# Kernel optimization log

Hardware: AMD Instinct MI355X
Metric: run time of the kernel (lower is better)

The kernel has to match this reference:

```python
import jax, jax.numpy as jnp
import numpy as np

T, K, E, D, F = 2048, 6, 32, 2048, 1408   # tokens, top_k, routed experts, dim, moe_inter_dim
S = 2                                      # fused shared experts
C = T * K // E                             # exact per-expert capacity (balanced routing)


def _silu_and_mul(gu):
    # merged gate_up activation: silu(gate_half) * up_half
    g, u = jnp.split(gu, 2, axis=-1)
    return jax.nn.silu(g) * u


def setup_inputs() -> dict:
    key = jax.random.key(0)
    ks = jax.random.split(key, 7)
    x = jax.random.normal(ks[0], (T, D), dtype=jnp.float32)
    # balanced routing: every expert receives exactly C = T*K/E token-expert pairs
    indices = jax.random.permutation(ks[1], jnp.arange(T * K, dtype=jnp.int32) % E).reshape(T, K)
    weights = jax.random.uniform(ks[2], (T, K), dtype=jnp.float32)
    scale = 0.02
    w_gate_up = jax.random.normal(ks[3], (E, D, 2 * F), dtype=jnp.float32) * scale
    w_down = jax.random.normal(ks[4], (E, F, D), dtype=jnp.float32) * scale
    w_gate_up_shared = jax.random.normal(ks[5], (S, D, 2 * F), dtype=jnp.float32) * scale
    w_down_shared = jax.random.normal(ks[6], (S, F, D), dtype=jnp.float32) * scale
    return {"x": x, "weights": weights, "w_gate_up": w_gate_up, "w_down": w_down,
            "w_gate_up_shared": w_gate_up_shared, "w_down_shared": w_down_shared,
            "indices": indices}


def reference(x, weights, w_gate_up, w_down, w_gate_up_shared, w_down_shared, indices):
    # ---- dispatch: sort token-expert pairs by expert id (balanced -> exactly C per expert)
    flat_e = indices.reshape(-1)                       # [T*K]
    order = jnp.argsort(flat_e, stable=True)           # [T*K] pair ids grouped by expert
    tok = order // K                                   # source token of each sorted pair
    w_sorted = weights.reshape(-1)[order]              # routing weight of each sorted pair
    xg = x[tok].reshape(E, C, D)                       # gathered per-expert inputs
    # ---- routed experts: grouped gate_up GEMM -> silu_and_mul -> down GEMM
    act = _silu_and_mul(jnp.einsum('ecd,edf->ecf', xg, w_gate_up))   # [E, C, F]
    down = jnp.einsum('ecf,efd->ecd', act, w_down)                   # [E, C, D]
    # ---- combine: weighted scatter-add back to token order (y[idx] += out * weights[idx, top])
    y = jnp.zeros_like(x).at[tok].add(down.reshape(E * C, D) * w_sorted[:, None])
    # ---- fused shared experts: run on all tokens, added unweighted
    act_s = _silu_and_mul(jnp.einsum('td,sdf->stf', x, w_gate_up_shared))  # [S, T, F]
    y = y + jnp.einsum('stf,sfd->td', act_s, w_down_shared)
    return y
```

## Files before the change

### kernel.cpp

```cpp
#include <hip/hip_runtime.h>
#include <hip/hip_bf16.h>

#define TT 2048
#define KK 6
#define EE 32
#define DD 2048
#define FF 1408
#define SS 2
#define CC 384

typedef __bf16 bf16_t;
typedef __attribute__((ext_vector_type(8))) __bf16 bf16x8;
typedef __attribute__((ext_vector_type(4))) float f32x4;
typedef unsigned int u32;

#define AS1 __attribute__((address_space(1)))
#define AS3 __attribute__((address_space(3)))

__device__ __forceinline__ u32 f2bf(float f) {
    u32 u = __builtin_bit_cast(u32, f);
    return (u + 0x7fffu + ((u >> 16) & 1u)) >> 16;
}
__device__ __forceinline__ u32 pack2(float a, float b) {
    return f2bf(a) | (f2bf(b) << 16);
}
__device__ __forceinline__ float silu_mul(float g, float u) {
    return (g / (1.0f + __expf(-g))) * u;
}

__global__ void k_dispatch(const int* __restrict__ idx, int* __restrict__ counts,
                           int* __restrict__ tok, int* __restrict__ sop) {
    int p = blockIdx.x * 256 + threadIdx.x;
    if (p >= TT * KK) return;
    int e = idx[p];
    int pos = atomicAdd(&counts[e], 1);
    int slot = e * CC + pos;
    tok[slot] = p / KK;
    sop[p] = slot;
}

__global__ void k_gather(const float* __restrict__ x, const int* __restrict__ tok,
                         bf16_t* __restrict__ xall) {
    int row = blockIdx.x;
    int srow = (row < EE * CC) ? tok[row] : (row - EE * CC);
    const float* src = x + (size_t)srow * DD;
    bf16_t* dst = xall + (size_t)row * DD;
    int c0 = threadIdx.x * 8;
    float4 a = *(const float4*)(src + c0);
    float4 b = *(const float4*)(src + c0 + 4);
    uint4 o;
    o.x = pack2(a.x, a.y); o.y = pack2(a.z, a.w);
    o.z = pack2(b.x, b.y); o.w = pack2(b.z, b.w);
    *(uint4*)(dst + c0) = o;
}

template<bool FUSED>
__global__ __launch_bounds__(512) void k_gemm_r(
    const bf16_t* __restrict__ Aall, const float* __restrict__ Br,
    bf16_t* __restrict__ Out, int Kdim, int Bstr, int Ostr, int NB)
{
    const int lin = blockIdx.x;
    const int xcd = lin & 7, jj = lin >> 3;
    const int e = xcd + 8 * (jj / NB);
    const int nblk = jj % NB;

    const bf16_t* A = Aall + (size_t)e * CC * Kdim;
    const float* Bbase = Br + (size_t)e * Kdim * Bstr;

    const int tid = threadIdx.x;
    const int lane = tid & 63, wid = tid >> 6;
    const int m_base = (wid >> 1) * 96, wn = wid & 1;
    const int l15 = lane & 15, lq = lane >> 4;
    const int arow8 = tid >> 3, achunk = tid & 7;
    const int bn = tid & 127, kb = (tid >> 7) * 16;

    const float* bsrc;
    bf16_t* Cout;
    if (FUSED) {
        bsrc = Bbase + ((bn & 64) ? FF : 0) + nblk * 64 + (bn & 63);
        Cout = Out + (size_t)e * CC * Ostr + nblk * 64;
    } else {
        bsrc = Bbase + nblk * 128 + bn;
        Cout = Out + (size_t)e * CC * Ostr + nblk * 128;
    }

    __shared__ __align__(16) bf16_t As[2][384 * 64];
    __shared__ __align__(16) bf16_t Bs[2][128 * 72];

    f32x4 acc[6][4] = {};
    const int ks = Kdim >> 6;

    auto stageA = [&](int kt, bf16_t* dst) {
        const int k0 = kt << 6;
        #pragma unroll
        for (int i = 0; i < 6; ++i) {
            const int row = i * 64 + arow8;
            const int c = achunk ^ (row & 7);
            const bf16_t* g = A + (size_t)row * Kdim + (k0 + c * 8);
            AS3 u32* l = (AS3 u32*)(void*)(dst + (size_t)(i * 64 + wid * 8) * 64);
            __builtin_amdgcn_global_load_lds((const AS1 u32*)(const void*)g, l, 16, 0, 0);
        }
    };
    auto loadB = [&](int kt, float* v) {
        const float* sp = bsrc + (size_t)((kt << 6) + kb) * Bstr;
        #pragma unroll
        for (int t = 0; t < 16; ++t) v[t] = sp[(size_t)t * Bstr];
    };
    auto writeB = [&](bf16_t* bbuf, const float* v) {
        uint4 w0, w1;
        w0.x = pack2(v[0], v[1]);   w0.y = pack2(v[2], v[3]);
        w0.z = pack2(v[4], v[5]);   w0.w = pack2(v[6], v[7]);
        w1.x = pack2(v[8], v[9]);   w1.y = pack2(v[10], v[11]);
        w1.z = pack2(v[12], v[13]); w1.w = pack2(v[14], v[15]);
        *(uint4*)(bbuf + (size_t)bn * 72 + kb) = w0;
        *(uint4*)(bbuf + (size_t)bn * 72 + kb + 8) = w1;
    };
    auto compute = [&](const bf16_t* abuf, const bf16_t* bbuf) {
        __builtin_amdgcn_s_setprio(1);
        #pragma unroll
        for (int kh = 0; kh < 2; ++kh) {
            bf16x8 bfr[4];
            #pragma unroll
            for (int j = 0; j < 4; ++j) {
                const int n_ds = FUSED ? (wn * 32 + (j & 1) * 16 + (j >> 1) * 64)
                                       : (wn * 64 + j * 16);
                bfr[j] = *(const bf16x8*)(bbuf + (size_t)(n_ds + l15) * 72 + kh * 32 + lq * 8);
            }
            #pragma unroll
            for (int m = 0; m < 6; ++m) {
                const int row = m_base + m * 16 + l15;
                bf16x8 af = *(const bf16x8*)(abuf + (size_t)row * 64
                               + (size_t)(((kh * 4 + lq) ^ (row & 7)) * 8));
                #pragma unroll
                for (int j = 0; j < 4; ++j)
                    acc[m][j] = __builtin_amdgcn_mfma_f32_16x16x32_bf16(af, bfr[j], acc[m][j], 0, 0, 0);
            }
        }
        __builtin_amdgcn_s_setprio(0);
    };

    float vBa[16], vBb[16];

    loadB(0, vBa);
    asm volatile("s_waitcnt vmcnt(0)" ::: "memory");
    writeB(&Bs[0][0], vBa);
    loadB(1, vBb);
    stageA(0, &As[0][0]);
    asm volatile("s_waitcnt lgkmcnt(0)" ::: "memory");
    __builtin_amdgcn_s_barrier();

    for (int t = 0; t < ks - 2; t += 2) {
        loadB(t + 2, vBa);
        asm volatile("s_waitcnt vmcnt(16)" ::: "memory");
        asm volatile("s_waitcnt lgkmcnt(0)" ::: "memory");
        __builtin_amdgcn_s_barrier();
        stageA(t + 1, &As[1][0]);
        compute(&As[0][0], &Bs[0][0]);
        writeB(&Bs[1][0], vBb);
        loadB(t + 3, vBb);
        asm volatile("s_waitcnt vmcnt(16)" ::: "memory");
        asm volatile("s_waitcnt lgkmcnt(0)" ::: "memory");
        __builtin_amdgcn_s_barrier();
        stageA(t + 2, &As[0][0]);
        compute(&As[1][0], &Bs[1][0]);
        writeB(&Bs[0][0], vBa);
    }

    asm volatile("s_waitcnt vmcnt(0)" ::: "memory");
    asm volatile("s_waitcnt lgkmcnt(0)" ::: "memory");
    __builtin_amdgcn_s_barrier();
    stageA(ks - 1, &As[1][0]);
    compute(&As[0][0], &Bs[0][0]);
    writeB(&Bs[1][0], vBb);
    asm volatile("s_waitcnt vmcnt(0)" ::: "memory");
    asm volatile("s_waitcnt lgkmcnt(0)" ::: "memory");
    __builtin_amdgcn_s_barrier();
    compute(&As[1][0], &Bs[1][0]);

    if (FUSED) {
        #pragma unroll
        for (int m = 0; m < 6; ++m)
            #pragma unroll
            for (int j = 0; j < 2; ++j) {
                const int n = wn * 32 + j * 16 + l15;
                #pragma unroll
                for (int r = 0; r < 4; ++r) {
                    const int mm = m_base + m * 16 + lq * 4 + r;
                    Cout[(size_t)mm * Ostr + n] = (bf16_t)silu_mul(acc[m][j][r], acc[m][j + 2][r]);
                }
            }
    } else {
        #pragma unroll
        for (int m = 0; m < 6; ++m)
            #pragma unroll
            for (int j = 0; j < 4; ++j) {
                const int n = wn * 64 + j * 16 + l15;
                #pragma unroll
                for (int r = 0; r < 4; ++r) {
                    const int mm = m_base + m * 16 + lq * 4 + r;
                    Cout[(size_t)mm * Ostr + n] = (bf16_t)acc[m][j][r];
                }
            }
    }
}

#define BSTR 40
template<bool FUSED>
__global__ __launch_bounds__(256) void k_gemm_s(
    const bf16_t* __restrict__ Ash, const float* __restrict__ Bsh,
    bf16_t* __restrict__ Out, int Kdim, int Bstr, int Ostr, int ash_stride,
    int nkeys, int KQ, int NBs)
{
    const int b = blockIdx.x;
    const int xcd = b & 7, jj = b >> 3;
    const int m = jj / KQ, kq = jj % KQ;
    const int key = kq * 8 + xcd;
    if (key >= nkeys) return;
    const int s = key / NBs, nb = key % NBs;

    const bf16_t* A = Ash + ((size_t)s * ash_stride + (size_t)m * 128) * Kdim;
    const float* Bp = Bsh + (size_t)s * Kdim * Bstr;

    const int tid = threadIdx.x;
    const int lane = tid & 63, wid = tid >> 6;
    const int m_off = (wid >> 1) * 64, wn = wid & 1;
    const int l15 = lane & 15, lq = lane >> 4;
    const int arow = tid >> 2, ac = tid & 3;
    const int bn = tid & 127, kb = (tid >> 7) * 16;

    const float* bsrc;
    bf16_t* Cout;
    if (FUSED) {
        bsrc = Bp + (((tid >> 6) & 1) ? FF : 0) + nb * 64 + (tid & 63);
        Cout = Out + ((size_t)s * TT + (size_t)m * 128) * Ostr + nb * 64;
    } else {
        bsrc = Bp + nb * 128 + bn;
        Cout = Out + ((size_t)s * TT + (size_t)m * 128) * Ostr + nb * 128;
    }

    __shared__ __align__(16) bf16_t As[3][128 * 32];
    __shared__ __align__(16) bf16_t Bs[2][128 * BSTR];

    f32x4 acc[4][4] = {};
    const int ksteps = Kdim >> 5;

    auto stageA = [&](int kt, bf16_t* dst) {
        const int k0 = kt << 5;
        #pragma unroll
        for (int i = 0; i < 2; ++i) {
            const int row = i * 64 + arow;
            const int cs = ac ^ ((row >> 1) & 3);
            const bf16_t* g = A + (size_t)row * Kdim + (k0 + cs * 8);
            AS3 u32* l = (AS3 u32*)(void*)(dst + (size_t)(i * 64 + wid * 16) * 32);
            __builtin_amdgcn_global_load_lds((const AS1 u32*)(const void*)g, l, 16, 0, 0);
        }
    };
    auto loadB = [&](int kt, float* v) {
        const float* sp = bsrc + (size_t)((kt << 5) + kb) * Bstr;
        #pragma unroll
        for (int t = 0; t < 16; ++t) v[t] = sp[(size_t)t * Bstr];
    };
    auto writeB = [&](bf16_t* bbuf, const float* v) {
        u32 p[8];
        #pragma unroll
        for (int t = 0; t < 8; ++t) p[t] = pack2(v[2 * t], v[2 * t + 1]);
        uint4 w0, w1;
        w0.x = p[0]; w0.y = p[1]; w0.z = p[2]; w0.w = p[3];
        w1.x = p[4]; w1.y = p[5]; w1.z = p[6]; w1.w = p[7];
        *(uint4*)(bbuf + (size_t)bn * BSTR + kb) = w0;
        *(uint4*)(bbuf + (size_t)bn * BSTR + kb + 8) = w1;
    };
    auto compute = [&](const bf16_t* abuf, const bf16_t* bbuf) {
        bf16x8 af[4], bfr[4];
        #pragma unroll
        for (int i = 0; i < 4; ++i) {
            const int row = m_off + i * 16 + l15;
            af[i] = *(const bf16x8*)(abuf + (size_t)row * 32 + (size_t)((lq ^ ((row >> 1) & 3)) * 8));
        }
        #pragma unroll
        for (int j = 0; j < 4; ++j) {
            const int n_ds = FUSED ? (wn * 32 + (j & 1) * 16 + (j >> 1) * 64)
                                   : (wn * 64 + j * 16);
            bfr[j] = *(const bf16x8*)(bbuf + (size_t)(n_ds + l15) * BSTR + lq * 8);
        }
        #pragma unroll
        for (int i = 0; i < 4; ++i)
            #pragma unroll
            for (int j = 0; j < 4; ++j)
                acc[i][j] = __builtin_amdgcn_mfma_f32_16x16x32_bf16(af[i], bfr[j], acc[i][j], 0, 0, 0);
    };

    float vBa[16], vBb[16];
    bf16_t *aR = &As[0][0], *aS = &As[1][0], *aT = &As[2][0];

    loadB(0, vBa);
    stageA(0, aR);
    asm volatile("s_waitcnt vmcnt(2)" ::: "memory");
    writeB(&Bs[0][0], vBa);
    loadB(1, vBb);
    stageA(1, aS);
    asm volatile("s_waitcnt lgkmcnt(0)" ::: "memory");
    __builtin_amdgcn_s_barrier();

    for (int t = 0; t < ksteps - 2; t += 2) {
        loadB(t + 2, vBa);
        asm volatile("s_waitcnt vmcnt(34)" ::: "memory");
        asm volatile("s_waitcnt lgkmcnt(0)" ::: "memory");
        __builtin_amdgcn_s_barrier();
        stageA(t + 2, aT);
        compute(aR, &Bs[0][0]);
        asm volatile("s_waitcnt vmcnt(20)" ::: "memory");
        writeB(&Bs[1][0], vBb);
        { bf16_t* tmp = aR; aR = aS; aS = aT; aT = tmp; }
        loadB(t + 3, vBb);
        asm volatile("s_waitcnt vmcnt(34)" ::: "memory");
        asm volatile("s_waitcnt lgkmcnt(0)" ::: "memory");
        __builtin_amdgcn_s_barrier();
        stageA(t + 3, aT);
        compute(aR, &Bs[1][0]);
        asm volatile("s_waitcnt vmcnt(20)" ::: "memory");
        writeB(&Bs[0][0], vBa);
        { bf16_t* tmp = aR; aR = aS; aS = aT; aT = tmp; }
    }

    asm volatile("s_waitcnt vmcnt(18)" ::: "memory");
    asm volatile("s_waitcnt lgkmcnt(0)" ::: "memory");
    __builtin_amdgcn_s_barrier();
    compute(aR, &Bs[0][0]);
    asm volatile("s_waitcnt vmcnt(2)" ::: "memory");
    writeB(&Bs[1][0], vBb);
    asm volatile("s_waitcnt vmcnt(0)" ::: "memory");
    asm volatile("s_waitcnt lgkmcnt(0)" ::: "memory");
    __builtin_amdgcn_s_barrier();
    compute(aS, &Bs[1][0]);

    if (FUSED) {
        #pragma unroll
        for (int i = 0; i < 4; ++i)
            #pragma unroll
            for (int j = 0; j < 2; ++j) {
                const int n = wn * 32 + j * 16 + l15;
                #pragma unroll
                for (int r = 0; r < 4; ++r) {
                    const int mm = m_off + i * 16 + lq * 4 + r;
                    Cout[(size_t)mm * Ostr + n] = (bf16_t)silu_mul(acc[i][j][r], acc[i][j + 2][r]);
                }
            }
    } else {
        #pragma unroll
        for (int i = 0; i < 4; ++i)
            #pragma unroll
            for (int j = 0; j < 4; ++j) {
                const int n = wn * 64 + j * 16 + l15;
                #pragma unroll
                for (int r = 0; r < 4; ++r) {
                    const int mm = m_off + i * 16 + lq * 4 + r;
                    Cout[(size_t)mm * Ostr + n] = (bf16_t)acc[i][j][r];
                }
            }
    }
}

__global__ void k_combine(const bf16_t* __restrict__ down, const int* __restrict__ sop,
                          const float* __restrict__ wts, float* __restrict__ y) {
    int t = blockIdx.x;
    int d0 = threadIdx.x * 8;
    float a[8] = {0, 0, 0, 0, 0, 0, 0, 0};
    #pragma unroll
    for (int k = 0; k < KK; ++k) {
        int slot = sop[t * KK + k];
        float w = wts[t * KK + k];
        bf16x8 v = *(const bf16x8*)(down + (size_t)slot * DD + d0);
        #pragma unroll
        for (int j = 0; j < 8; ++j) a[j] += w * (float)v[j];
    }
    #pragma unroll
    for (int s = 0; s < SS; ++s) {
        bf16x8 v = *(const bf16x8*)(down + ((size_t)EE * CC + (size_t)s * TT + t) * DD + d0);
        #pragma unroll
        for (int j = 0; j < 8; ++j) a[j] += (float)v[j];
    }
    float4 o0, o1;
    o0.x = a[0]; o0.y = a[1]; o0.z = a[2]; o0.w = a[3];
    o1.x = a[4]; o1.y = a[5]; o1.z = a[6]; o1.w = a[7];
    *(float4*)(y + (size_t)t * DD + d0) = o0;
    *(float4*)(y + (size_t)t * DD + d0 + 4) = o1;
}

extern "C" void kernel_launch(void* const* d_in, const int* in_sizes, int n_in,
                              void* d_out, int out_size, void* d_ws, size_t ws_size,
                              hipStream_t stream) {
    (void)in_sizes; (void)n_in; (void)out_size; (void)ws_size;
    const float* x      = (const float*)d_in[0];
    const float* wts    = (const float*)d_in[1];
    const float* w_gu   = (const float*)d_in[2];
    const float* w_dn   = (const float*)d_in[3];
    const float* w_gu_s = (const float*)d_in[4];
    const float* w_dn_s = (const float*)d_in[5];
    const int*   indices= (const int*)d_in[6];
    float* y = (float*)d_out;

    char* ws = (char*)d_ws;
    size_t off = 0;
    auto alloc = [&](size_t bytes) {
        void* p = ws + off;
        off = (off + bytes + 255) & ~(size_t)255;
        return p;
    };
    int*    counts = (int*)alloc((size_t)EE * 4);
    int*    tok    = (int*)alloc((size_t)EE * CC * 4);
    int*    sop    = (int*)alloc((size_t)TT * KK * 4);
    bf16_t* xall   = (bf16_t*)alloc((size_t)(EE * CC + TT) * DD * 2);
    bf16_t* actb   = (bf16_t*)alloc((size_t)(EE * CC + SS * TT) * FF * 2);
    bf16_t* dnout  = (bf16_t*)alloc((size_t)(EE * CC + SS * TT) * DD * 2);

    hipMemsetAsync(counts, 0, EE * 4, stream);
    k_dispatch<<<(TT * KK + 255) / 256, 256, 0, stream>>>(indices, counts, tok, sop);
    k_gather<<<EE * CC + TT, 256, 0, stream>>>(x, tok, xall);

    k_gemm_r<true><<<EE * 22, 512, 0, stream>>>(xall, w_gu, actb, DD, 2 * FF, FF, 22);
    k_gemm_s<true><<<8 * 6 * 16, 256, 0, stream>>>(
        xall + (size_t)EE * CC * DD, w_gu_s, actb + (size_t)EE * CC * FF,
        DD, 2 * FF, FF, 0, 44, 6, 22);

    k_gemm_r<false><<<EE * 16, 512, 0, stream>>>(actb, w_dn, dnout, FF, DD, DD, 16);
    k_gemm_s<false><<<8 * 4 * 16, 256, 0, stream>>>(
        actb + (size_t)EE * CC * FF, w_dn_s, dnout + (size_t)EE * CC * DD,
        FF, DD, DD, TT, 32, 4, 16);

    k_combine<<<TT, 256, 0, stream>>>(dnout, sop, wts, y);
}
```

Baseline: 1.490 ms.

## Vectorize fp32 weight loads with float2, swizzle B LDS, split silu into separate kernel

```diff
diff --git a/kernel.cpp b/kernel.cpp
--- a/kernel.cpp
+++ b/kernel.cpp
@@ -16,6 +16,9 @@
 
 #define AS1 __attribute__((address_space(1)))
 #define AS3 __attribute__((address_space(3)))
+
+#define SWZB8(n) (((((n) >> 1) & 7)) ^ (((((n) >> 4) & 1)) << 2))
+#define SWZB4(n) (((((n) >> 1) & 3)) ^ ((((n) >> 3) & 3)))
 
 __device__ __forceinline__ u32 f2bf(float f) {
     u32 u = __builtin_bit_cast(u32, f);
@@ -54,7 +57,6 @@
     *(uint4*)(dst + c0) = o;
 }
 
-template<bool FUSED>
 __global__ __launch_bounds__(512) void k_gemm_r(
     const bf16_t* __restrict__ Aall, const float* __restrict__ Br,
     bf16_t* __restrict__ Out, int Kdim, int Bstr, int Ostr, int NB)
@@ -72,17 +74,10 @@
     const int m_base = (wid >> 1) * 96, wn = wid & 1;
     const int l15 = lane & 15, lq = lane >> 4;
     const int arow8 = tid >> 3, achunk = tid & 7;
-    const int bn = tid & 127, kb = (tid >> 7) * 16;
-
-    const float* bsrc;
-    bf16_t* Cout;
-    if (FUSED) {
-        bsrc = Bbase + ((bn & 64) ? FF : 0) + nblk * 64 + (bn & 63);
-        Cout = Out + (size_t)e * CC * Ostr + nblk * 64;
-    } else {
-        bsrc = Bbase + nblk * 128 + bn;
-        Cout = Out + (size_t)e * CC * Ostr + nblk * 128;
-    }
+    const int n2 = lane * 2;
+
+    const float* bsrc = Bbase + nblk * 128 + n2;
+    bf16_t* Cout = Out + (size_t)e * CC * Ostr + nblk * 128;
 
     __shared__ __align__(16) bf16_t As[2][384 * 64];
     __shared__ __align__(16) bf16_t Bs[2][128 * 72];
@@ -101,19 +96,20 @@
             __builtin_amdgcn_global_load_lds((const AS1 u32*)(const void*)g, l, 16, 0, 0);
         }
     };
-    auto loadB = [&](int kt, float* v) {
-        const float* sp = bsrc + (size_t)((kt << 6) + kb) * Bstr;
-        #pragma unroll
-        for (int t = 0; t < 16; ++t) v[t] = sp[(size_t)t * Bstr];
-    };
-    auto writeB = [&](bf16_t* bbuf, const float* v) {
-        uint4 w0, w1;
-        w0.x = pack2(v[0], v[1]);   w0.y = pack2(v[2], v[3]);
-        w0.z = pack2(v[4], v[5]);   w0.w = pack2(v[6], v[7]);
-        w1.x = pack2(v[8], v[9]);   w1.y = pack2(v[10], v[11]);
-        w1.z = pack2(v[12], v[13]); w1.w = pack2(v[14], v[15]);
-        *(uint4*)(bbuf + (size_t)bn * 72 + kb) = w0;
-        *(uint4*)(bbuf + (size_t)bn * 72 + kb + 8) = w1;
+    auto loadB = [&](int kt, float2* v) {
+        const float* sp = bsrc + (size_t)((kt << 6) + wid * 8) * Bstr;
+        #pragma unroll
+        for (int p = 0; p < 8; ++p) v[p] = *(const float2*)(sp + (size_t)p * Bstr);
+    };
+    auto writeB = [&](bf16_t* bbuf, const float2* v) {
+        uint4 wa, wb;
+        wa.x = pack2(v[0].x, v[1].x); wa.y = pack2(v[2].x, v[3].x);
+        wa.z = pack2(v[4].x, v[5].x); wa.w = pack2(v[6].x, v[7].x);
+        wb.x = pack2(v[0].y, v[1].y); wb.y = pack2(v[2].y, v[3].y);
+        wb.z = pack2(v[4].y, v[5].y); wb.w = pack2(v[6].y, v[7].y);
+        const int c = (wid ^ SWZB8(n2)) * 8;
+        *(uint4*)(bbuf + (size_t)n2 * 72 + c) = wa;
+        *(uint4*)(bbuf + (size_t)(n2 + 1) * 72 + c) = wb;
     };
     auto compute = [&](const bf16_t* abuf, const bf16_t* bbuf) {
         __builtin_amdgcn_s_setprio(1);
@@ -122,9 +118,9 @@
             bf16x8 bfr[4];
             #pragma unroll
             for (int j = 0; j < 4; ++j) {
-                const int n_ds = FUSED ? (wn * 32 + (j & 1) * 16 + (j >> 1) * 64)
-                                       : (wn * 64 + j * 16);
-                bfr[j] = *(const bf16x8*)(bbuf + (size_t)(n_ds + l15) * 72 + kh * 32 + lq * 8);
+                const int n = wn * 64 + j * 16 + l15;
+                bfr[j] = *(const bf16x8*)(bbuf + (size_t)n * 72
+                            + (size_t)(((kh * 4 + lq) ^ SWZB8(n)) * 8));
             }
             #pragma unroll
             for (int m = 0; m < 6; ++m) {
@@ -139,7 +135,7 @@
         __builtin_amdgcn_s_setprio(0);
     };
 
-    float vBa[16], vBb[16];
+    float2 vBa[8], vBb[8];
 
     loadB(0, vBa);
     asm volatile("s_waitcnt vmcnt(0)" ::: "memory");
@@ -151,14 +147,14 @@
 
     for (int t = 0; t < ks - 2; t += 2) {
         loadB(t + 2, vBa);
-        asm volatile("s_waitcnt vmcnt(16)" ::: "memory");
+        asm volatile("s_waitcnt vmcnt(8)" ::: "memory");
         asm volatile("s_waitcnt lgkmcnt(0)" ::: "memory");
         __builtin_amdgcn_s_barrier();
         stageA(t + 1, &As[1][0]);
         compute(&As[0][0], &Bs[0][0]);
         writeB(&Bs[1][0], vBb);
         loadB(t + 3, vBb);
-        asm volatile("s_waitcnt vmcnt(16)" ::: "memory");
+        asm volatile("s_waitcnt vmcnt(8)" ::: "memory");
         asm volatile("s_waitcnt lgkmcnt(0)" ::: "memory");
         __builtin_amdgcn_s_barrier();
         stageA(t + 2, &As[0][0]);
@@ -177,34 +173,19 @@
     __builtin_amdgcn_s_barrier();
     compute(&As[1][0], &Bs[1][0]);
 
-    if (FUSED) {
-        #pragma unroll
-        for (int m = 0; m < 6; ++m)
-            #pragma unroll
-            for (int j = 0; j < 2; ++j) {
-                const int n = wn * 32 + j * 16 + l15;
-                #pragma unroll
-                for (int r = 0; r < 4; ++r) {
-                    const int mm = m_base + m * 16 + lq * 4 + r;
-                    Cout[(size_t)mm * Ostr + n] = (bf16_t)silu_mul(acc[m][j][r], acc[m][j + 2][r]);
-                }
+    #pragma unroll
+    for (int m = 0; m < 6; ++m)
+        #pragma unroll
+        for (int j = 0; j < 4; ++j) {
+            const int n = wn * 64 + j * 16 + l15;
+            #pragma unroll
+            for (int r = 0; r < 4; ++r) {
+                const int mm = m_base + m * 16 + lq * 4 + r;
+                Cout[(size_t)mm * Ostr + n] = (bf16_t)acc[m][j][r];
             }
-    } else {
-        #pragma unroll
-        for (int m = 0; m < 6; ++m)
-            #pragma unroll
-            for (int j = 0; j < 4; ++j) {
-                const int n = wn * 64 + j * 16 + l15;
-                #pragma unroll
-                for (int r = 0; r < 4; ++r) {
-                    const int mm = m_base + m * 16 + lq * 4 + r;
-                    Cout[(size_t)mm * Ostr + n] = (bf16_t)acc[m][j][r];
-                }
-            }
-    }
-}
-
-#define BSTR 40
+        }
+}
+
 template<bool FUSED>
 __global__ __launch_bounds__(256) void k_gemm_s(
     const bf16_t* __restrict__ Ash, const float* __restrict__ Bsh,
@@ -226,20 +207,20 @@
     const int m_off = (wid >> 1) * 64, wn = wid & 1;
     const int l15 = lane & 15, lq = lane >> 4;
     const int arow = tid >> 2, ac = tid & 3;
-    const int bn = tid & 127, kb = (tid >> 7) * 16;
+    const int n2 = lane * 2;
 
     const float* bsrc;
     bf16_t* Cout;
     if (FUSED) {
-        bsrc = Bp + (((tid >> 6) & 1) ? FF : 0) + nb * 64 + (tid & 63);
+        bsrc = Bp + ((n2 & 64) ? (FF + nb * 64 + (n2 & 63)) : (nb * 64 + n2));
         Cout = Out + ((size_t)s * TT + (size_t)m * 128) * Ostr + nb * 64;
     } else {
-        bsrc = Bp + nb * 128 + bn;
+        bsrc = Bp + nb * 128 + n2;
         Cout = Out + ((size_t)s * TT + (size_t)m * 128) * Ostr + nb * 128;
     }
 
     __shared__ __align__(16) bf16_t As[3][128 * 32];
-    __shared__ __align__(16) bf16_t Bs[2][128 * BSTR];
+    __shared__ __align__(16) bf16_t Bs[2][128 * 40];
 
     f32x4 acc[4][4] = {};
     const int ksteps = Kdim >> 5;
@@ -255,20 +236,20 @@
             __builtin_amdgcn_global_load_lds((const AS1 u32*)(const void*)g, l, 16, 0, 0);
         }
     };
-    auto loadB = [&](int kt, float* v) {
-        const float* sp = bsrc + (size_t)((kt << 5) + kb) * Bstr;
-        #pragma unroll
-        for (int t = 0; t < 16; ++t) v[t] = sp[(size_t)t * Bstr];
-    };
-    auto writeB = [&](bf16_t* bbuf, const float* v) {
-        u32 p[8];
-        #pragma unroll
-        for (int t = 0; t < 8; ++t) p[t] = pack2(v[2 * t], v[2 * t + 1]);
-        uint4 w0, w1;
-        w0.x = p[0]; w0.y = p[1]; w0.z = p[2]; w0.w = p[3];
-        w1.x = p[4]; w1.y = p[5]; w1.z = p[6]; w1.w = p[7];
-        *(uint4*)(bbuf + (size_t)bn * BSTR + kb) = w0;
-        *(uint4*)(bbuf + (size_t)bn * BSTR + kb + 8) = w1;
+    auto loadB = [&](int kt, float2* v) {
+        const float* sp = bsrc + (size_t)((kt << 5) + wid * 8) * Bstr;
+        #pragma unroll
+        for (int p = 0; p < 8; ++p) v[p] = *(const float2*)(sp + (size_t)p * Bstr);
+    };
+    auto writeB = [&](bf16_t* bbuf, const float2* v) {
+        uint4 wa, wb;
+        wa.x = pack2(v[0].x, v[1].x); wa.y = pack2(v[2].x, v[3].x);
+        wa.z = pack2(v[4].x, v[5].x); wa.w = pack2(v[6].x, v[7].x);
+        wb.x = pack2(v[0].y, v[1].y); wb.y = pack2(v[2].y, v[3].y);
+        wb.z = pack2(v[4].y, v[5].y); wb.w = pack2(v[6].y, v[7].y);
+        const int c = (wid ^ SWZB4(n2)) * 8;
+        *(uint4*)(bbuf + (size_t)n2 * 40 + c) = wa;
+        *(uint4*)(bbuf + (size_t)(n2 + 1) * 40 + c) = wb;
     };
     auto compute = [&](const bf16_t* abuf, const bf16_t* bbuf) {
         bf16x8 af[4], bfr[4];
@@ -281,7 +262,8 @@
         for (int j = 0; j < 4; ++j) {
             const int n_ds = FUSED ? (wn * 32 + (j & 1) * 16 + (j >> 1) * 64)
                                    : (wn * 64 + j * 16);
-            bfr[j] = *(const bf16x8*)(bbuf + (size_t)(n_ds + l15) * BSTR + lq * 8);
+            const int n = n_ds + l15;
+            bfr[j] = *(const bf16x8*)(bbuf + (size_t)n * 40 + (size_t)((lq ^ SWZB4(n)) * 8));
         }
         #pragma unroll
         for (int i = 0; i < 4; ++i)
@@ -290,7 +272,7 @@
                 acc[i][j] = __builtin_amdgcn_mfma_f32_16x16x32_bf16(af[i], bfr[j], acc[i][j], 0, 0, 0);
     };
 
-    float vBa[16], vBb[16];
+    float2 vBa[8], vBb[8];
     bf16_t *aR = &As[0][0], *aS = &As[1][0], *aT = &As[2][0];
 
     loadB(0, vBa);
@@ -304,26 +286,26 @@
 
     for (int t = 0; t < ksteps - 2; t += 2) {
         loadB(t + 2, vBa);
-        asm volatile("s_waitcnt vmcnt(34)" ::: "memory");
+        asm volatile("s_waitcnt vmcnt(18)" ::: "memory");
         asm volatile("s_waitcnt lgkmcnt(0)" ::: "memory");
         __builtin_amdgcn_s_barrier();
         stageA(t + 2, aT);
         compute(aR, &Bs[0][0]);
-        asm volatile("s_waitcnt vmcnt(20)" ::: "memory");
+        asm volatile("s_waitcnt vmcnt(12)" ::: "memory");
         writeB(&Bs[1][0], vBb);
         { bf16_t* tmp = aR; aR = aS; aS = aT; aT = tmp; }
         loadB(t + 3, vBb);
-        asm volatile("s_waitcnt vmcnt(34)" ::: "memory");
+        asm volatile("s_waitcnt vmcnt(18)" ::: "memory");
         asm volatile("s_waitcnt lgkmcnt(0)" ::: "memory");
         __builtin_amdgcn_s_barrier();
         stageA(t + 3, aT);
         compute(aR, &Bs[1][0]);
-        asm volatile("s_waitcnt vmcnt(20)" ::: "memory");
+        asm volatile("s_waitcnt vmcnt(12)" ::: "memory");
         writeB(&Bs[0][0], vBa);
         { bf16_t* tmp = aR; aR = aS; aS = aT; aT = tmp; }
     }
 
-    asm volatile("s_waitcnt vmcnt(18)" ::: "memory");
+    asm volatile("s_waitcnt vmcnt(10)" ::: "memory");
     asm volatile("s_waitcnt lgkmcnt(0)" ::: "memory");
     __builtin_amdgcn_s_barrier();
     compute(aR, &Bs[0][0]);
@@ -359,6 +341,22 @@
                 }
             }
     }
+}
+
+__global__ void k_silu(const bf16_t* __restrict__ gu, bf16_t* __restrict__ act) {
+    u32 f = ((u32)blockIdx.x * 256 + threadIdx.x) * 8;
+    u32 row = f / FF;
+    u32 col = f % FF;
+    const bf16_t* base = gu + (size_t)row * (2 * FF) + col;
+    bf16x8 g = *(const bf16x8*)(base);
+    bf16x8 u = *(const bf16x8*)(base + FF);
+    bf16x8 ov;
+    #pragma unroll
+    for (int j = 0; j < 8; ++j) {
+        float gf = (float)g[j], uf = (float)u[j];
+        ov[j] = (bf16_t)silu_mul(gf, uf);
+    }
+    *(bf16x8*)(act + (size_t)row * FF + col) = ov;
 }
 
 __global__ void k_combine(const bf16_t* __restrict__ down, const int* __restrict__ sop,
@@ -411,6 +409,7 @@
     int*    tok    = (int*)alloc((size_t)EE * CC * 4);
     int*    sop    = (int*)alloc((size_t)TT * KK * 4);
     bf16_t* xall   = (bf16_t*)alloc((size_t)(EE * CC + TT) * DD * 2);
+    bf16_t* gu     = (bf16_t*)alloc((size_t)EE * CC * 2 * FF * 2);
     bf16_t* actb   = (bf16_t*)alloc((size_t)(EE * CC + SS * TT) * FF * 2);
     bf16_t* dnout  = (bf16_t*)alloc((size_t)(EE * CC + SS * TT) * DD * 2);
 
@@ -418,12 +417,13 @@
     k_dispatch<<<(TT * KK + 255) / 256, 256, 0, stream>>>(indices, counts, tok, sop);
     k_gather<<<EE * CC + TT, 256, 0, stream>>>(x, tok, xall);
 
-    k_gemm_r<true><<<EE * 22, 512, 0, stream>>>(xall, w_gu, actb, DD, 2 * FF, FF, 22);
+    k_gemm_r<<<EE * 22, 512, 0, stream>>>(xall, w_gu, gu, DD, 2 * FF, 2 * FF, 22);
     k_gemm_s<true><<<8 * 6 * 16, 256, 0, stream>>>(
         xall + (size_t)EE * CC * DD, w_gu_s, actb + (size_t)EE * CC * FF,
         DD, 2 * FF, FF, 0, 44, 6, 22);
-
-    k_gemm_r<false><<<EE * 16, 512, 0, stream>>>(actb, w_dn, dnout, FF, DD, DD, 16);
+    k_silu<<<(EE * CC) * FF / 8 / 256, 256, 0, stream>>>(gu, actb);
+
+    k_gemm_r<<<EE * 16, 512, 0, stream>>>(actb, w_dn, dnout, FF, DD, DD, 16);
     k_gemm_s<false><<<8 * 4 * 16, 256, 0, stream>>>(
         actb + (size_t)EE * CC * FF, w_dn_s, dnout + (size_t)EE * CC * DD,
         FF, DD, DD, TT, 32, 4, 16);
```

Measured after the change: 1.516 ms. No clear change (+1.7%).
